# Optimization experiments

Hardware: AMD Instinct MI355X
Metric: run time of the kernel (lower is better)

Reference implementation:

```python
import jax, jax.numpy as jnp
import numpy as np
import math

B = 1024      # graphs
N = 64        # nodes per graph (padded, masked by node_mask)
BN = B * N    # total nodes
EPG = 192     # directed edges per graph
E = B * EPG


def setup_inputs() -> dict:
    key = jax.random.key(0)
    ks = jax.random.split(key, 40)

    def nrm(k, shp, s=0.02):
        return (jax.random.normal(k, shp) * s).astype(jnp.float32)

    mol_batch_x = jax.random.normal(ks[0], (BN, 19), dtype=jnp.float32)
    offs = jnp.arange(B, dtype=jnp.int32) * N
    src = jax.random.randint(ks[1], (B, EPG), 0, N, dtype=jnp.int32) + offs[:, None]
    dst = jax.random.randint(ks[2], (B, EPG), 0, N, dtype=jnp.int32) + offs[:, None]
    mol_batch_edge_index = jnp.stack([src.reshape(-1), dst.reshape(-1)], axis=0)
    mol_batch_batch = jnp.repeat(jnp.arange(B, dtype=jnp.int32), N)
    text_features = jax.random.normal(ks[3], (B, 300), dtype=jnp.float32)
    timesteps = jax.random.uniform(ks[4], (B,), minval=0.0, maxval=1000.0, dtype=jnp.float32)
    node_mask = (jax.random.uniform(ks[5], (B, N)) > 0.1).astype(jnp.float32)

    p = {
        'W_tr': nrm(ks[6], (19, 300)),   'b_tr': jnp.zeros((300,), jnp.float32),
        'W_c1': nrm(ks[7], (300, 600)),  'b_c1': jnp.zeros((600,), jnp.float32),
        'W_c2': nrm(ks[8], (600, 600)),  'b_c2': jnp.zeros((600,), jnp.float32),
        'W_c3': nrm(ks[9], (600, 600)),  'b_c3': jnp.zeros((600,), jnp.float32),
        'W_h1': nrm(ks[10], (600, 600)), 'b_h1': jnp.zeros((600,), jnp.float32),
        'W_h2': nrm(ks[11], (600, 600)), 'b_h2': jnp.zeros((600,), jnp.float32),
        'W_h3': nrm(ks[12], (600, 300)), 'b_h3': jnp.zeros((300,), jnp.float32),
        'ln_g': jnp.ones((300,), jnp.float32), 'ln_b': jnp.zeros((300,), jnp.float32),
        'W_t1': nrm(ks[13], (128, 512)), 'b_t1': jnp.zeros((512,), jnp.float32),
        'W_t2': nrm(ks[14], (512, 512)), 'b_t2': jnp.zeros((512,), jnp.float32),
        'W_e':  nrm(ks[15], (512, 3000)), 'b_e': jnp.zeros((3000,), jnp.float32),
    }
    return dict(mol_batch_x=mol_batch_x, mol_batch_edge_index=mol_batch_edge_index,
                mol_batch_batch=mol_batch_batch, text_features=text_features,
                timesteps=timesteps, node_mask=node_mask, **p)


def timestep_embedding(t, dim=128, max_period=10000.0):
    half = dim // 2
    freqs = jnp.exp(-math.log(max_period) * jnp.arange(half, dtype=jnp.float32) / half)
    args = t[:, None] * freqs[None]                 # [B, half]
    return jnp.concatenate([jnp.cos(args), jnp.sin(args)], axis=-1)  # [B, dim]


def gcn_conv(x, W, b, src, dst, num_nodes):
    # PyG GCNConv: D^{-1/2} (A + I) D^{-1/2} X W + b, edge weights 1
    h = x @ W                                             # [BN, F]
    deg = jnp.zeros((num_nodes,), h.dtype).at[dst].add(1.0) + 1.0  # in-degree + self-loop
    inv_sqrt = jax.lax.rsqrt(deg)
    coef = inv_sqrt[src] * inv_sqrt[dst]                  # [E]
    agg = jax.ops.segment_sum(h[src] * coef[:, None], dst, num_segments=num_nodes)
    return agg + h * (1.0 / deg)[:, None] + b             # self-loop norm = 1/deg


def global_mean_pool(x, batch, num_graphs):
    sums = jax.ops.segment_sum(x, batch, num_segments=num_graphs)
    cnts = jax.ops.segment_sum(jnp.ones((x.shape[0],), x.dtype), batch, num_segments=num_graphs)
    return sums / jnp.maximum(cnts, 1.0)[:, None]


def layer_norm(x, g, b, eps=1e-5):
    mu = jnp.mean(x, axis=-1, keepdims=True)
    var = jnp.mean(jnp.square(x - mu), axis=-1, keepdims=True)
    return (x - mu) * jax.lax.rsqrt(var + eps) * g + b


def reference(mol_batch_x, mol_batch_edge_index, mol_batch_batch, text_features,
              timesteps, node_mask, W_tr, b_tr, W_c1, b_c1, W_c2, b_c2, W_c3, b_c3,
              W_h1, b_h1, W_h2, b_h2, W_h3, b_h3, ln_g, ln_b,
              W_t1, b_t1, W_t2, b_t2, W_e, b_e):
    num_nodes = mol_batch_x.shape[0]
    num_graphs = node_mask.shape[0]
    src, dst = mol_batch_edge_index[0], mol_batch_edge_index[1]

    # FiLM conditioning from timestep embedding
    emb = jax.nn.relu(timestep_embedding(timesteps, 128) @ W_t1 + b_t1) @ W_t2 + b_t2  # [B,512]
    emb_out = jax.nn.relu(emb) @ W_e + b_e                                             # [B,3000]
    s1, t1 = emb_out[:, 0:600], emb_out[:, 600:1200]
    s2, t2 = emb_out[:, 1200:1800], emb_out[:, 1800:2400]
    s3, t3 = emb_out[:, 2400:2700], emb_out[:, 2700:3000]

    # node transform + mask
    x = mol_batch_x @ W_tr + b_tr                     # [BN, 300]
    x = x * node_mask.reshape(-1, 1)

    # GCN stack
    x = jax.nn.relu(gcn_conv(x, W_c1, b_c1, src, dst, num_nodes))
    x = jax.nn.relu(gcn_conv(x, W_c2, b_c2, src, dst, num_nodes))
    x = gcn_conv(x, W_c3, b_c3, src, dst, num_nodes)  # [BN, 600]

    g = global_mean_pool(x, mol_batch_batch, num_graphs)  # [B, 600]
    g = jax.nn.relu(g @ W_h1 + b_h1)
    g = g * (1.0 + s1) + t1
    g = jax.nn.relu(g @ W_h2 + b_h2)
    g = g * (1.0 + s2) + t2
    g = g @ W_h3 + b_h3                                # [B, 300]
    g = g * (1.0 + s3) + t3
    g = layer_norm(g, ln_g, ln_b)
    return (g, text_features)
```

## Files before the change

### kernel.cpp

```cpp
#include <hip/hip_runtime.h>
#include <hip/hip_bf16.h>
#include <cstdint>
#include <cstddef>

static constexpr int B   = 1024;
static constexpr int N   = 64;
static constexpr int BN  = B * N;
static constexpr int EPG = 192;
static constexpr int E   = B * EPG;
static constexpr int FP  = 608;
static constexpr int KP1 = 320;
static constexpr int PMS = 72;
static constexpr int NCONV = 2560;

typedef __hip_bfloat16 bf16;
typedef __bf16 bf16x8 __attribute__((ext_vector_type(8)));
typedef __bf16 bf16x4 __attribute__((ext_vector_type(4)));
typedef float  f32x4  __attribute__((ext_vector_type(4)));

__device__ __forceinline__ void storeC(float* p, float v) { *p = v; }
__device__ __forceinline__ void storeC(bf16* p, float v) { *p = __float2bfloat16(v); }

__device__ __forceinline__ void llds16(const void* g, void* l) {
    __builtin_amdgcn_global_load_lds(
        (const __attribute__((address_space(1))) unsigned int*)g,
        (__attribute__((address_space(3))) unsigned int*)l,
        16, 0, 0);
}


template<bool RELU, bool FILM, typename CT>
__device__ __forceinline__ void g64_tile(
    const bf16* __restrict__ A, int lda,
    const bf16* __restrict__ Bt, int ldb,
    const float* __restrict__ bias,
    CT* __restrict__ C, int ldc, int Ncap,
    const bf16* __restrict__ fS, const bf16* __restrict__ fT, int fstride,
    int K, int m0, int n0, char* lds, int tid)
{
    const int lane = tid & 63;
    const int w    = tid >> 6;
    const int wn   = w * 32;
    const int l15  = lane & 15;
    const int lhi  = lane >> 4;
    const int co   = (lhi ^ ((l15 >> 1) & 3)) << 3;
    const int nk   = K >> 5;

    auto stage = [&](int k0, char* buf) {
        {
            int row = tid >> 2;
            int kc  = (tid & 3) ^ ((row >> 1) & 3);
            llds16(A + (size_t)(m0 + row) * lda + k0 + kc * 8,
                   buf + (size_t)(w * 64) * 16);
        }
        #pragma unroll
        for (int t = 0; t < 2; ++t) {
            int ci  = t * 256 + tid;
            int row = ci >> 2;
            int kc  = (ci & 3) ^ ((row >> 1) & 3);
            llds16(Bt + (size_t)(n0 + row) * ldb + k0 + kc * 8,
                   buf + 4096 + (size_t)(t * 256 + w * 64) * 16);
        }
    };

    f32x4 acc[4][2] = {};
    stage(0, lds);
    asm volatile("s_waitcnt vmcnt(0)" ::: "memory");
    __syncthreads();

    for (int k = 0; k < nk; ++k) {
        if (k + 1 < nk) stage((k + 1) << 5, lds + ((k + 1) & 1) * 12288);

        __bf16* As = (__bf16*)(lds + (k & 1) * 12288);
        __bf16* Bs = As + 2048;
        bf16x8 af[4], bg[2];
        #pragma unroll
        for (int i = 0; i < 4; ++i)
            af[i] = *(bf16x8*)(As + (i * 16 + l15) * 32 + co);
        #pragma unroll
        for (int j = 0; j < 2; ++j)
            bg[j] = *(bf16x8*)(Bs + (wn + j * 16 + l15) * 32 + co);
        #pragma unroll
        for (int i = 0; i < 4; ++i)
            #pragma unroll
            for (int j = 0; j < 2; ++j)
                acc[i][j] = __builtin_amdgcn_mfma_f32_16x16x32_bf16(
                    af[i], bg[j], acc[i][j], 0, 0, 0);

        asm volatile("s_waitcnt vmcnt(0)" ::: "memory");
        __syncthreads();
    }

    #pragma unroll
    for (int i = 0; i < 4; ++i) {
        #pragma unroll
        for (int j = 0; j < 2; ++j) {
            int col = n0 + wn + j * 16 + l15;
            if (col < Ncap) {
                float bv = bias ? bias[col] : 0.f;
                #pragma unroll
                for (int e = 0; e < 4; ++e) {
                    int row = m0 + i * 16 + lhi * 4 + e;
                    float v = acc[i][j][e] + bv;
                    if (RELU) v = fmaxf(v, 0.f);
                    if (FILM) {
                        float sv = __bfloat162float(fS[(size_t)row * fstride + col]);
                        float tv = __bfloat162float(fT[(size_t)row * fstride + col]);
                        v = v * (1.f + sv) + tv;
                    }
                    storeC(&C[(size_t)row * ldc + col], v);
                }
            }
        }
    }
}

__device__ __forceinline__ void g64_tile8(
    const bf16* __restrict__ A, int lda,
    const bf16* __restrict__ Bt, int ldb,
    const float* __restrict__ bias,
    bf16* __restrict__ C, int ldc, int Ncap,
    int K, int m0, int n0, char* lds, int tid)
{
    const int lane = tid & 63;
    const int w    = tid >> 6;
    const int wn   = w * 16;
    const int l15  = lane & 15;
    const int lhi  = lane >> 4;
    const int co   = (lhi ^ ((l15 >> 1) & 3)) << 3;
    const int nk   = K >> 5;

    auto stage = [&](int k0, char* buf) {
        if (tid < 256) {
            int row = tid >> 2;
            int kc  = (tid & 3) ^ ((row >> 1) & 3);
            llds16(A + (size_t)(m0 + row) * lda + k0 + kc * 8,
                   buf + (size_t)(w * 64) * 16);
        }
        {
            int row = tid >> 2;
            int kc  = (tid & 3) ^ ((row >> 1) & 3);
            llds16(Bt + (size_t)(n0 + row) * ldb + k0 + kc * 8,
                   buf + 4096 + (size_t)(w * 64) * 16);
        }
    };

    f32x4 acc[4] = {};
    stage(0, lds);
    asm volatile("s_waitcnt vmcnt(0)" ::: "memory");
    __syncthreads();

    for (int k = 0; k < nk; ++k) {
        if (k + 1 < nk) stage((k + 1) << 5, lds + ((k + 1) & 1) * 12288);

        __bf16* As = (__bf16*)(lds + (k & 1) * 12288);
        __bf16* Bs = As + 2048;
        bf16x8 af[4], bg;
        #pragma unroll
        for (int i = 0; i < 4; ++i)
            af[i] = *(bf16x8*)(As + (i * 16 + l15) * 32 + co);
        bg = *(bf16x8*)(Bs + (wn + l15) * 32 + co);
        #pragma unroll
        for (int i = 0; i < 4; ++i)
            acc[i] = __builtin_amdgcn_mfma_f32_16x16x32_bf16(af[i], bg, acc[i], 0, 0, 0);

        asm volatile("s_waitcnt vmcnt(0)" ::: "memory");
        __syncthreads();
    }

    int col = n0 + wn + l15;
    if (col < Ncap) {
        float bv = bias ? bias[col] : 0.f;
        #pragma unroll
        for (int i = 0; i < 4; ++i)
            #pragma unroll
            for (int e = 0; e < 4; ++e) {
                int row = m0 + i * 16 + lhi * 4 + e;
                float v = fmaxf(acc[i][e] + bv, 0.f);
                C[(size_t)row * ldc + col] = __float2bfloat16(v);
            }
    }
}

__device__ __attribute__((noinline)) void guest_g64(
    const bf16* gA, int glda, const bf16* gBt, int gldb,
    const float* gbias, bf16* gC, int gldc, int gNcap, int gK, int gnt,
    int t, char* lds, int tid)
{
    int mt2 = t / gnt, nt2 = t % gnt;
    g64_tile8(gA, glda, gBt, gldb, gbias, gC, gldc, gNcap,
              gK, mt2 * 64, nt2 * 128, lds, tid);
}

template<bool RELU, bool FILM, typename CT>
__global__ __launch_bounds__(256) void gemm64(
    const bf16* __restrict__ A, int lda,
    const bf16* __restrict__ Bt, int ldb,
    const float* __restrict__ bias,
    CT* __restrict__ C, int ldc, int Ncap,
    const bf16* __restrict__ fS, const bf16* __restrict__ fT, int fstride,
    int K)
{
    __shared__ __align__(16) char lds[24576];
    g64_tile<RELU, FILM, CT>(A, lda, Bt, ldb, bias, C, ldc, Ncap,
                             fS, fT, fstride, K,
                             blockIdx.x * 64, blockIdx.y * 128, lds,
                             threadIdx.x);
}

__global__ __launch_bounds__(256) void k_two_gemms(
    const bf16* __restrict__ A2b, const bf16* __restrict__ Wet,
    const float* __restrict__ b_e, bf16* __restrict__ EO,
    const bf16* __restrict__ Yv, const bf16* __restrict__ Wb3,
    const float* __restrict__ b_c3, bf16* __restrict__ G0)
{
    __shared__ __align__(16) char lds[24576];
    int bid = blockIdx.x;
    if (bid < 384) {
        int mt = bid / 24, nt = bid % 24;
        g64_tile<false, false, bf16>(A2b, 512, Wet, 512, b_e, EO, 3000, 3000,
                                     nullptr, nullptr, 0, 512,
                                     mt * 64, nt * 128, lds, threadIdx.x);
    } else {
        int t = bid - 384;
        int mt = t / 5, nt = t % 5;
        g64_tile<false, false, bf16>(Yv, FP, Wb3, FP, b_c3, G0, FP, 600,
                                     nullptr, nullptr, 0, FP,
                                     mt * 64, nt * 128, lds, threadIdx.x);
    }
}

__global__ __launch_bounds__(512, 6) void conv1_gemm(
    const bf16* __restrict__ A,
    const bf16* __restrict__ Bt,
    const float* __restrict__ bias,
    bf16* __restrict__ X1,
    const bf16* __restrict__ gA, int glda,
    const bf16* __restrict__ gBt, int gldb,
    const float* __restrict__ gbias,
    bf16* __restrict__ gC, int gldc, int gNcap, int gK, int gnt)
{
    __shared__ __align__(16) char regA[32768];
    const int tid = threadIdx.x;
    const int bid = blockIdx.x;

    if (bid >= NCONV) {
        guest_g64(gA, glda, gBt, gldb, gbias, gC, gldc, gNcap, gK, gnt,
                  bid - NCONV, regA, tid);
        return;
    }

    const int lane = tid & 63;
    const int w    = tid >> 6;
    const int wm   = (w & 1) * 64;
    const int wn   = (w >> 1) * 32;
    const int l15  = lane & 15;
    const int lhi  = lane >> 4;
    const int co   = (lhi ^ ((l15 >> 1) & 3)) << 3;

    const int lid = bid >> 3;
    const int mt  = (bid & 7) * 64 + lid / 5;
    const int nt  = lid % 5;
    const int m0  = mt * 128;
    const int n0  = nt * 128;

    auto stage = [&](int k0, char* buf) {
        int row = tid >> 2;
        int kc  = (tid & 3) ^ ((row >> 1) & 3);
        llds16(A  + (size_t)(m0 + row) * KP1 + k0 + kc * 8,
               buf + (size_t)(w * 64) * 16);
        llds16(Bt + (size_t)(n0 + row) * KP1 + k0 + kc * 8,
               buf + 8192 + (size_t)(w * 64) * 16);
    };

    constexpr int nk = KP1 / 32;
    f32x4 acc[4][2] = {};
    stage(0, regA);
    asm volatile("s_waitcnt vmcnt(0)" ::: "memory");
    __syncthreads();

    for (int k = 0; k < nk; ++k) {
        if (k + 1 < nk) stage((k + 1) << 5, regA + ((k + 1) & 1) * 16384);

        __bf16* As = (__bf16*)(regA + (k & 1) * 16384);
        __bf16* Bs = As + 4096;
        bf16x8 af[4], bg[2];
        #pragma unroll
        for (int i = 0; i < 4; ++i)
            af[i] = *(bf16x8*)(As + (wm + i * 16 + l15) * 32 + co);
        #pragma unroll
        for (int j = 0; j < 2; ++j)
            bg[j] = *(bf16x8*)(Bs + (wn + j * 16 + l15) * 32 + co);
        #pragma unroll
        for (int i = 0; i < 4; ++i)
            #pragma unroll
            for (int j = 0; j < 2; ++j)
                acc[i][j] = __builtin_amdgcn_mfma_f32_16x16x32_bf16(
                    af[i], bg[j], acc[i][j], 0, 0, 0);

        asm volatile("s_waitcnt vmcnt(0)" ::: "memory");
        __syncthreads();
    }

    #pragma unroll
    for (int i = 0; i < 4; ++i)
        #pragma unroll
        for (int j = 0; j < 2; ++j) {
            int col = n0 + wn + j * 16 + l15;
            if (col < FP) {
                float bv = (col < 600) ? bias[col] : 0.f;
                #pragma unroll
                for (int e = 0; e < 4; ++e) {
                    int row = m0 + wm + i * 16 + lhi * 4 + e;
                    float v = fmaxf(acc[i][j][e] + bv, 0.f);
                    X1[(size_t)row * FP + col] = __float2bfloat16(v);
                }
            }
        }
}

__global__ __launch_bounds__(512, 6) void conv_fused_q(
    const bf16* __restrict__ A, int lda, int K,
    const bf16* __restrict__ Bt, int ldb,
    const bf16* __restrict__ Pmg,
    const float* __restrict__ bias,
    const float* __restrict__ qv,
    bf16* __restrict__ Y,
    const bf16* __restrict__ gA, int glda,
    const bf16* __restrict__ gBt, int gldb,
    const float* __restrict__ gbias,
    bf16* __restrict__ gC, int gldc, int gNcap, int gK, int gnt)
{
    __shared__ __align__(16) char regA[35840];
    __shared__ float s_q[128];

    const int tid = threadIdx.x;
    const int bid = blockIdx.x;

    if (bid >= NCONV) {
        guest_g64(gA, glda, gBt, gldb, gbias, gC, gldc, gNcap, gK, gnt,
                  bid - NCONV, regA, tid);
        return;
    }

    __bf16* Ts = (__bf16*)regA;
    __bf16* Pm = (__bf16*)(regA + 17408);

    const int lane = tid & 63;
    const int w    = tid >> 6;
    const int wm   = (w & 1) * 64;
    const int wn   = (w >> 1) * 32;
    const int l15  = lane & 15;
    const int lhi  = lane >> 4;
    const int co   = (lhi ^ ((l15 >> 1) & 3)) << 3;

    const int lid = bid >> 3;
    const int mt  = (bid & 7) * 64 + lid / 5;
    const int nt  = lid % 5;
    const int m0  = mt * 128;
    const int n0  = nt * 128;

    if (tid < 128) s_q[tid] = qv[mt * 128 + tid];

    auto stage = [&](int k0, char* buf) {
        int row = tid >> 2;
        int kc  = (tid & 3) ^ ((row >> 1) & 3);
        llds16(A  + (size_t)(m0 + row) * lda + k0 + kc * 8,
               buf + (size_t)(w * 64) * 16);
        llds16(Bt + (size_t)(n0 + row) * ldb + k0 + kc * 8,
               buf + 8192 + (size_t)(w * 64) * 16);
    };

    const int nk = K >> 5;
    f32x4 acc[4][2] = {};
    stage(0, regA);
    asm volatile("s_waitcnt vmcnt(0)" ::: "memory");
    __syncthreads();

    for (int k = 0; k < nk; ++k) {
        if (k + 1 < nk) {
            stage((k + 1) << 5, regA + ((k + 1) & 1) * 16384);
        } else {
            #pragma unroll
            for (int i = 0; i < 2; ++i)
                llds16(Pmg + (size_t)mt * (128 * PMS) + (size_t)(i * 512 + tid) * 8,
                       (char*)Pm + (size_t)(i * 512 + w * 64) * 16);
            if (w < 2)
                llds16(Pmg + (size_t)mt * (128 * PMS) + (size_t)(1024 + w * 64 + lane) * 8,
                       (char*)Pm + (size_t)(1024 + w * 64) * 16);
        }

        __bf16* As = (__bf16*)(regA + (k & 1) * 16384);
        __bf16* Bs = As + 4096;
        bf16x8 af[4], bg[2];
        #pragma unroll
        for (int i = 0; i < 4; ++i)
            af[i] = *(bf16x8*)(As + (wm + i * 16 + l15) * 32 + co);
        #pragma unroll
        for (int j = 0; j < 2; ++j)
            bg[j] = *(bf16x8*)(Bs + (wn + j * 16 + l15) * 32 + co);
        #pragma unroll
        for (int i = 0; i < 4; ++i)
            #pragma unroll
            for (int j = 0; j < 2; ++j)
                acc[i][j] = __builtin_amdgcn_mfma_f32_16x16x32_bf16(
                    af[i], bg[j], acc[i][j], 0, 0, 0);

        asm volatile("s_waitcnt vmcnt(0)" ::: "memory");
        __syncthreads();
    }

    const int g  = w & 1;
    const int nb = w >> 1;
    #pragma unroll
    for (int h = 0; h < 2; ++h) {
        if ((w >> 2) == h) {
            #pragma unroll
            for (int i = 0; i < 4; ++i)
                #pragma unroll
                for (int j = 0; j < 2; ++j) {
                    int c_local = (wn & 63) + j * 16 + l15;
                    int rbase   = wm + i * 16 + lhi * 4;
                    bf16x4 pk;
                    #pragma unroll
                    for (int e = 0; e < 4; ++e) pk[e] = (__bf16)acc[i][j][e];
                    *(bf16x4*)(Ts + c_local * 136 + rbase) = pk;
                }
        }
        __syncthreads();

        f32x4 acc2[4] = {};
        #pragma unroll
        for (int k0 = 0; k0 < 64; k0 += 32) {
            bf16x8 pa[4], hb;
            #pragma unroll
            for (int i = 0; i < 4; ++i)
                pa[i] = *(bf16x8*)(Pm + (g * 64 + i * 16 + l15) * PMS + k0 + lhi * 8);
            hb = *(bf16x8*)(Ts + (nb * 16 + l15) * 136 + g * 64 + k0 + lhi * 8);
            #pragma unroll
            for (int i = 0; i < 4; ++i)
                acc2[i] = __builtin_amdgcn_mfma_f32_16x16x32_bf16(
                    pa[i], hb, acc2[i], 0, 0, 0);
        }
        {
            int col = n0 + h * 64 + nb * 16 + l15;
            float bv = (col < 600) ? bias[col] : 0.f;
            float yp = 0.f;
            #pragma unroll
            for (int i = 0; i < 4; ++i)
                #pragma unroll
                for (int e = 0; e < 4; ++e) {
                    float v = fmaxf(acc2[i][e] + bv, 0.f);
                    yp += s_q[g * 64 + i * 16 + lhi * 4 + e] * v;
                }
            yp += __shfl_xor(yp, 16, 64);
            yp += __shfl_xor(yp, 32, 64);
            if (lhi == 0 && col < FP)
                Y[(size_t)(mt * 2 + g) * FP + col] = __float2bfloat16(yp);
        }
        __syncthreads();
    }
}

struct WtJob  { const float* src; bf16* dst; int Ksrc, Nsrc, Kp, Np, blk0; };
struct PrepArgs {
    WtJob j[9];
    int nwt, te0, pp0, xtr0;
    const int*   ei;
    const float* ts;
    const float* xin; const float* Wtr; const float* btr; const float* mask;
    bf16* TE; bf16* Pmg; float* qv; bf16* PX0;
};

__global__ __launch_bounds__(256) void k_prep(PrepArgs a)
{
    __shared__ __align__(16) char sm[35840];
    const int bx  = blockIdx.x;
    const int tid = threadIdx.x;

    if (bx < a.nwt) {
        int ji = 0;
        while (ji < 8 && bx >= a.j[ji + 1].blk0) ++ji;
        WtJob jb = a.j[ji];
        int t  = bx - jb.blk0;
        int kt = (jb.Kp + 63) >> 6;
        int ti = t % kt, tj = t / kt;
        int kg0 = ti * 64, ng0 = tj * 64;
        float (*T)[65] = (float(*)[65])sm;
        #pragma unroll 4
        for (int r = 0; r < 16; ++r) {
            int kl = (tid >> 6) + r * 4, nl = tid & 63;
            int kg = kg0 + kl, ng = ng0 + nl;
            T[kl][nl] = (kg < jb.Ksrc && ng < jb.Nsrc)
                        ? jb.src[(size_t)kg * jb.Nsrc + ng] : 0.f;
        }
        __syncthreads();
        #pragma unroll 4
        for (int r = 0; r < 16; ++r) {
            int nl = (tid >> 6) + r * 4, kl = tid & 63;
            int ng = ng0 + nl, kg = kg0 + kl;
            if (ng < jb.Np && kg < jb.Kp)
                jb.dst[(size_t)ng * jb.Kp + kg] = __float2bfloat16(T[kl][nl]);
        }
    } else if (bx < a.pp0) {
        int idx = (bx - a.te0) * 256 + tid;
        int b = idx >> 7, jj = idx & 127;
        float tt = a.ts[b];
        int h = jj & 63;
        float freq = expf(-9.210340371976184f * (float)h / 64.f);
        float ang = tt * freq;
        a.TE[idx] = __float2bfloat16((jj < 64) ? cosf(ang) : sinf(ang));
    } else if (bx < a.xtr0) {
        int pr = bx - a.pp0;
        float* Pf   = (float*)sm;
        int*   cnt  = (int*)(sm + 32768);
        float* sQ   = (float*)(sm + 33280);
        float* sI   = (float*)(sm + 33792);
        float* sIvd = (float*)(sm + 34304);

        for (int idx = tid; idx < 8192; idx += 256) Pf[idx] = 0.f;
        if (tid < 128) cnt[tid] = 0;
        __syncthreads();
        for (int e = tid; e < 2 * EPG; e += 256) {
            int g  = (e >= EPG);
            int eg = (2 * pr + g) * EPG + (e - g * EPG);
            int ld = (a.ei[E + eg] & 63) + g * 64;
            atomicAdd(&cnt[ld], 1);
        }
        __syncthreads();
        if (tid < 128) {
            float d = (float)cnt[tid] + 1.0f;
            float iv = 1.f / d;
            sIvd[tid] = iv;
            sI[tid]   = rsqrtf(d);
            sQ[tid]   = iv;
        }
        __syncthreads();
        for (int e = tid; e < 2 * EPG; e += 256) {
            int g   = (e >= EPG);
            int eg  = (2 * pr + g) * EPG + (e - g * EPG);
            int lsl = a.ei[eg] & 63;
            int ldl = a.ei[E + eg] & 63;
            float cf = sI[g * 64 + lsl] * sI[g * 64 + ldl];
            atomicAdd(&Pf[(g * 64 + ldl) * 64 + lsl], cf);
            atomicAdd(&sQ[g * 64 + lsl], cf);
        }
        __syncthreads();
        if (tid < 128) {
            Pf[tid * 64 + (tid & 63)] += sIvd[tid];
            a.qv[pr * 128 + tid] = sQ[tid] * (1.f / 64.f);
        }
        __syncthreads();
        for (int idx = tid; idx < 128 * PMS; idx += 256) {
            int r = idx / PMS, k = idx - r * PMS;
            float v = (k < 64) ? Pf[r * 64 + k] : 0.f;
            a.Pmg[(size_t)pr * (128 * PMS) + idx] = __float2bfloat16(v);
        }
    } else {
        int g = bx - a.xtr0;
        float* Pf  = (float*)sm;
        float* Ws  = (float*)sm;
        float* xm  = (float*)(sm + 23104);
        float* xa  = (float*)(sm + 28224);
        float* isqv= (float*)(sm + 33344);
        float* ivdv= (float*)(sm + 33600);
        int*   cnt = (int*)  (sm + 33856);
        float* sb  = (float*)(sm + 34112);

        for (int idx = tid; idx < 4096; idx += 256) Pf[idx] = 0.f;
        if (tid < 64) cnt[tid] = 0;
        __syncthreads();
        for (int e = tid; e < EPG; e += 256)
            atomicAdd(&cnt[a.ei[E + g * EPG + e] & 63], 1);
        __syncthreads();
        if (tid < 64) {
            float d = (float)cnt[tid] + 1.0f;
            ivdv[tid] = 1.f / d;
            isqv[tid] = rsqrtf(d);
        }
        __syncthreads();
        for (int e = tid; e < EPG; e += 256) {
            int ls = a.ei[g * EPG + e] & 63;
            int ld = a.ei[E + g * EPG + e] & 63;
            atomicAdd(&Pf[ld * 64 + ls], isqv[ls] * isqv[ld]);
        }
        for (int idx = tid; idx < 64 * 20; idx += 256) {
            int n = idx / 20, j = idx - n * 20;
            float mv = a.mask[g * 64 + n];
            xm[idx] = (j < 19) ? mv * a.xin[(size_t)(g * 64 + n) * 19 + j] : mv;
        }
        __syncthreads();
        if (tid < 64) Pf[tid * 64 + tid] += ivdv[tid];
        __syncthreads();
        for (int idx = tid; idx < 64 * 20; idx += 256) {
            int r = idx / 20, j = idx - r * 20;
            float s = 0.f;
            #pragma unroll 8
            for (int s2 = 0; s2 < 64; ++s2)
                s += Pf[r * 64 + s2] * xm[s2 * 20 + j];
            xa[idx] = s;
        }
        __syncthreads();
        for (int idx = tid; idx < 19 * 304; idx += 256) {
            int k = idx / 304, c = idx - k * 304;
            Ws[idx] = (c < 300) ? a.Wtr[k * 300 + c] : 0.f;
        }
        for (int c = tid; c < 304; c += 256)
            sb[c] = (c < 300) ? a.btr[c] : 0.f;
        __syncthreads();
        int n  = tid >> 2;
        int c0 = tid & 3;
        float ba = xa[n * 20 + 19];
        for (int c = c0; c < 304; c += 4) {
            float acc = ba * sb[c];
            #pragma unroll
            for (int k = 0; k < 19; ++k)
                acc += xa[n * 20 + k] * Ws[k * 304 + c];
            a.PX0[(size_t)(g * 64 + n) * KP1 + c] = __float2bfloat16(acc);
        }
        bf16x8 z = {};
        for (int idx = tid; idx < 64 * 2; idx += 256) {
            int nn = idx >> 1, jv = idx & 1;
            *(bf16x8*)((__bf16*)a.PX0 + (size_t)(g * 64 + nn) * KP1 + 304 + jv * 8) = z;
        }
    }
}

__global__ __launch_bounds__(256) void k_ln_copy(const float* __restrict__ G,
                                                 const float* __restrict__ lg,
                                                 const float* __restrict__ lb,
                                                 const float* __restrict__ text,
                                                 float* __restrict__ out)
{
    int r = blockIdx.x;
    int tid = threadIdx.x;
    __shared__ float red[4];
    __shared__ float smu, svar;

    float v0 = (tid < 300) ? G[r * 300 + tid] : 0.f;
    float v1 = (tid + 256 < 300) ? G[r * 300 + tid + 256] : 0.f;
    float s = v0 + v1;
    #pragma unroll
    for (int o = 32; o > 0; o >>= 1) s += __shfl_down(s, o, 64);
    if ((tid & 63) == 0) red[tid >> 6] = s;
    __syncthreads();
    if (tid == 0) smu = (red[0] + red[1] + red[2] + red[3]) * (1.f / 300.f);
    __syncthreads();
    float mu = smu;
    float d0 = (tid < 300) ? v0 - mu : 0.f;
    float d1 = (tid + 256 < 300) ? v1 - mu : 0.f;
    s = d0 * d0 + d1 * d1;
    #pragma unroll
    for (int o = 32; o > 0; o >>= 1) s += __shfl_down(s, o, 64);
    if ((tid & 63) == 0) red[tid >> 6] = s;
    __syncthreads();
    if (tid == 0) svar = (red[0] + red[1] + red[2] + red[3]) * (1.f / 300.f);
    __syncthreads();
    float rstd = rsqrtf(svar + 1e-5f);
    if (tid < 300)
        out[r * 300 + tid] = d0 * rstd * lg[tid] + lb[tid];
    if (tid + 256 < 300)
        out[r * 300 + tid + 256] = d1 * rstd * lg[tid + 256] + lb[tid + 256];
    float* o2 = out + (size_t)B * 300;
    for (int c = tid; c < 300; c += 256)
        o2[(size_t)r * 300 + c] = text[(size_t)r * 300 + c];
}

extern "C" void kernel_launch(void* const* d_in, const int* in_sizes, int n_in,
                              void* d_out, int out_size, void* d_ws, size_t ws_size,
                              hipStream_t stream)
{
    const float* x_in  = (const float*)d_in[0];
    const int*   ei    = (const int*)d_in[1];
    const float* text  = (const float*)d_in[3];
    const float* tst   = (const float*)d_in[4];
    const float* mask  = (const float*)d_in[5];
    const float* W_tr  = (const float*)d_in[6];
    const float* b_tr  = (const float*)d_in[7];
    const float* W_c1  = (const float*)d_in[8];
    const float* b_c1  = (const float*)d_in[9];
    const float* W_c2  = (const float*)d_in[10];
    const float* b_c2  = (const float*)d_in[11];
    const float* W_c3  = (const float*)d_in[12];
    const float* b_c3  = (const float*)d_in[13];
    const float* W_h1  = (const float*)d_in[14];
    const float* b_h1  = (const float*)d_in[15];
    const float* W_h2  = (const float*)d_in[16];
    const float* b_h2  = (const float*)d_in[17];
    const float* W_h3  = (const float*)d_in[18];
    const float* b_h3  = (const float*)d_in[19];
    const float* ln_g  = (const float*)d_in[20];
    const float* ln_b  = (const float*)d_in[21];
    const float* W_t1  = (const float*)d_in[22];
    const float* b_t1  = (const float*)d_in[23];
    const float* W_t2  = (const float*)d_in[24];
    const float* b_t2  = (const float*)d_in[25];
    const float* W_e   = (const float*)d_in[26];
    const float* b_e   = (const float*)d_in[27];

    char* w = (char*)d_ws;
    size_t off = 0;
    auto carve = [&](size_t bytes) {
        void* p = w + off;
        off += (bytes + 255) & ~(size_t)255;
        return p;
    };
    bf16*  PX0    = (bf16*) carve((size_t)BN * KP1 * 2);
    bf16*  X1     = (bf16*) carve((size_t)BN * FP * 2);
    bf16*  Wb1    = (bf16*) carve((size_t)640 * KP1 * 2);
    bf16*  Wb2    = (bf16*) carve((size_t)640 * FP * 2);
    bf16*  Wb3    = (bf16*) carve((size_t)640 * FP * 2);
    bf16*  Wt1t   = (bf16*) carve((size_t)512 * 128 * 2);
    bf16*  Wt2t   = (bf16*) carve((size_t)512 * 512 * 2);
    bf16*  Wet    = (bf16*) carve((size_t)3072 * 512 * 2);
    bf16*  Wh1t   = (bf16*) carve((size_t)640 * FP * 2);
    bf16*  Wh2t   = (bf16*) carve((size_t)640 * FP * 2);
    bf16*  Wh3t   = (bf16*) carve((size_t)384 * FP * 2);
    bf16*  TE     = (bf16*) carve((size_t)B * 128 * 2);
    bf16*  A1b    = (bf16*) carve((size_t)B * 512 * 2);
    bf16*  A2b    = (bf16*) carve((size_t)B * 512 * 2);
    bf16*  EO     = (bf16*) carve((size_t)B * 3000 * 2);
    bf16*  Yv     = (bf16*) carve((size_t)B * FP * 2);
    bf16*  G0     = (bf16*) carve((size_t)B * FP * 2);
    bf16*  G1     = (bf16*) carve((size_t)B * FP * 2);
    bf16*  G2     = (bf16*) carve((size_t)B * FP * 2);
    float* G3     = (float*)carve((size_t)B * 300 * 4);
    bf16*  Pmg    = (bf16*) carve((size_t)512 * 128 * PMS * 2);
    float* qv     = (float*)carve((size_t)BN * 4);
    (void)ws_size; (void)in_sizes; (void)n_in; (void)out_size;

    float* out = (float*)d_out;

    PrepArgs pa;
    struct JD { const float* s; bf16* d; int Ks, Ns, Kp, Np; };
    JD jd[9] = {
        { W_c1, Wb1,  300, 600,  KP1, 640 },
        { W_c2, Wb2,  600, 600,  FP,  640 },
        { W_c3, Wb3,  600, 600,  FP,  640 },
        { W_t1, Wt1t, 128, 512,  128, 512 },
        { W_t2, Wt2t, 512, 512,  512, 512 },
        { W_e,  Wet,  512, 3000, 512, 3072 },
        { W_h1, Wh1t, 600, 600,  FP,  640 },
        { W_h2, Wh2t, 600, 600,  FP,  640 },
        { W_h3, Wh3t, 600, 300,  FP,  384 },
    };
    int cum = 0;
    for (int i = 0; i < 9; ++i) {
        int kt = (jd[i].Kp + 63) >> 6, nt = (jd[i].Np + 63) >> 6;
        pa.j[i] = { jd[i].s, jd[i].d, jd[i].Ks, jd[i].Ns, jd[i].Kp, jd[i].Np, cum };
        cum += kt * nt;
    }
    pa.nwt  = cum;
    pa.te0  = cum;       cum += (B * 128) / 256;
    pa.pp0  = cum;       cum += B / 2;
    pa.xtr0 = cum;       cum += B;
    pa.ei = ei; pa.ts = tst;
    pa.xin = x_in; pa.Wtr = W_tr; pa.btr = b_tr; pa.mask = mask;
    pa.TE = TE; pa.Pmg = Pmg; pa.qv = qv; pa.PX0 = PX0;
    k_prep<<<cum, 256, 0, stream>>>(pa);

    conv1_gemm<<<NCONV + 64, 512, 0, stream>>>(
        PX0, Wb1, b_c1, X1,
        TE, 128, Wt1t, 128, b_t1, A1b, 512, 512, 128, 4);

    conv_fused_q<<<NCONV + 64, 512, 0, stream>>>(
        X1, FP, FP, Wb2, FP, Pmg, b_c2, qv, Yv,
        A1b, 512, Wt2t, 512, b_t2, A2b, 512, 512, 512, 4);

    k_two_gemms<<<464, 256, 0, stream>>>(A2b, Wet, b_e, EO, Yv, Wb3, b_c3, G0);

    gemm64<true, true, bf16><<<dim3(16, 5), 256, 0, stream>>>(
        G0, FP, Wh1t, FP, b_h1, G1, FP, 600, EO + 0, EO + 600, 3000, FP);
    gemm64<true, true, bf16><<<dim3(16, 5), 256, 0, stream>>>(
        G1, FP, Wh2t, FP, b_h2, G2, FP, 600, EO + 1200, EO + 1800, 3000, FP);
    gemm64<false, true, float><<<dim3(16, 3), 256, 0, stream>>>(
        G2, FP, Wh3t, FP, b_h3, G3, 300, 300, EO + 2400, EO + 2700, 3000, FP);

    k_ln_copy<<<B, 256, 0, stream>>>(G3, ln_g, ln_b, text, out);
}
```

Before: 342.4 us.

## Widen conv GEMM tiles to 128x256 and prefetch propagation matrix upfront

The two conv GEMM kernels now use 128x256 output tiles instead of 128x128. Each wave computes a 64x64 sub-tile, and the grid shrinks from 2560 to 1536 conv blocks over three N-tiles. The propagation-matrix tile is loaded into its own LDS region at kernel start rather than during the last K iteration, and the conv1/conv2 weights are padded to 768 columns to match. The intent is to raise MFMA work per LDS load and cut redundant A-tile traffic, at the cost of larger LDS and register use, lower occupancy (launch bounds 6 to 4), and wasted compute on padded columns (768 vs 608).

```diff
diff --git a/kernel.cpp b/kernel.cpp
--- a/kernel.cpp
+++ b/kernel.cpp
@@ -11,7 +11,7 @@
 static constexpr int FP  = 608;
 static constexpr int KP1 = 320;
 static constexpr int PMS = 72;
-static constexpr int NCONV = 2560;
+static constexpr int NCONV = 1536;
 
 typedef __hip_bfloat16 bf16;
 typedef __bf16 bf16x8 __attribute__((ext_vector_type(8)));
@@ -230,7 +230,7 @@
     }
 }
 
-__global__ __launch_bounds__(512, 6) void conv1_gemm(
+__global__ __launch_bounds__(512, 4) void conv1_gemm(
     const bf16* __restrict__ A,
     const bf16* __restrict__ Bt,
     const float* __restrict__ bias,
@@ -240,7 +240,7 @@
     const float* __restrict__ gbias,
     bf16* __restrict__ gC, int gldc, int gNcap, int gK, int gnt)
 {
-    __shared__ __align__(16) char regA[32768];
+    __shared__ __align__(16) char regA[49152];
     const int tid = threadIdx.x;
     const int bid = blockIdx.x;
 
@@ -253,48 +253,58 @@
     const int lane = tid & 63;
     const int w    = tid >> 6;
     const int wm   = (w & 1) * 64;
-    const int wn   = (w >> 1) * 32;
+    const int wn   = (w >> 1) * 64;
     const int l15  = lane & 15;
     const int lhi  = lane >> 4;
     const int co   = (lhi ^ ((l15 >> 1) & 3)) << 3;
 
     const int lid = bid >> 3;
-    const int mt  = (bid & 7) * 64 + lid / 5;
-    const int nt  = lid % 5;
+    const int mt  = (bid & 7) * 64 + lid / 3;
+    const int nt  = lid % 3;
     const int m0  = mt * 128;
-    const int n0  = nt * 128;
+    const int n0  = nt * 256;
 
     auto stage = [&](int k0, char* buf) {
-        int row = tid >> 2;
-        int kc  = (tid & 3) ^ ((row >> 1) & 3);
-        llds16(A  + (size_t)(m0 + row) * KP1 + k0 + kc * 8,
-               buf + (size_t)(w * 64) * 16);
-        llds16(Bt + (size_t)(n0 + row) * KP1 + k0 + kc * 8,
-               buf + 8192 + (size_t)(w * 64) * 16);
+        #pragma unroll
+        for (int r = 0; r < 3; ++r) {
+            int ci = r * 512 + tid;
+            const bf16* src;
+            if (r == 0) {
+                int row = ci >> 2;
+                int kc  = (ci & 3) ^ ((row >> 1) & 3);
+                src = A + (size_t)(m0 + row) * KP1 + k0 + kc * 8;
+            } else {
+                int bi  = ci - 512;
+                int row = bi >> 2;
+                int kc  = (bi & 3) ^ ((row >> 1) & 3);
+                src = Bt + (size_t)(n0 + row) * KP1 + k0 + kc * 8;
+            }
+            llds16(src, buf + (size_t)(r * 512 + w * 64) * 16);
+        }
     };
 
     constexpr int nk = KP1 / 32;
-    f32x4 acc[4][2] = {};
+    f32x4 acc[4][4] = {};
     stage(0, regA);
     asm volatile("s_waitcnt vmcnt(0)" ::: "memory");
     __syncthreads();
 
     for (int k = 0; k < nk; ++k) {
-        if (k + 1 < nk) stage((k + 1) << 5, regA + ((k + 1) & 1) * 16384);
-
-        __bf16* As = (__bf16*)(regA + (k & 1) * 16384);
+        if (k + 1 < nk) stage((k + 1) << 5, regA + ((k + 1) & 1) * 24576);
+
+        __bf16* As = (__bf16*)(regA + (k & 1) * 24576);
         __bf16* Bs = As + 4096;
-        bf16x8 af[4], bg[2];
+        bf16x8 af[4], bg[4];
         #pragma unroll
         for (int i = 0; i < 4; ++i)
             af[i] = *(bf16x8*)(As + (wm + i * 16 + l15) * 32 + co);
         #pragma unroll
-        for (int j = 0; j < 2; ++j)
+        for (int j = 0; j < 4; ++j)
             bg[j] = *(bf16x8*)(Bs + (wn + j * 16 + l15) * 32 + co);
         #pragma unroll
         for (int i = 0; i < 4; ++i)
             #pragma unroll
-            for (int j = 0; j < 2; ++j)
+            for (int j = 0; j < 4; ++j)
                 acc[i][j] = __builtin_amdgcn_mfma_f32_16x16x32_bf16(
                     af[i], bg[j], acc[i][j], 0, 0, 0);
 
@@ -305,7 +315,7 @@
     #pragma unroll
     for (int i = 0; i < 4; ++i)
         #pragma unroll
-        for (int j = 0; j < 2; ++j) {
+        for (int j = 0; j < 4; ++j) {
             int col = n0 + wn + j * 16 + l15;
             if (col < FP) {
                 float bv = (col < 600) ? bias[col] : 0.f;
@@ -319,7 +329,7 @@
         }
 }
 
-__global__ __launch_bounds__(512, 6) void conv_fused_q(
+__global__ __launch_bounds__(512, 4) void conv_fused_q(
     const bf16* __restrict__ A, int lda, int K,
     const bf16* __restrict__ Bt, int ldb,
     const bf16* __restrict__ Pmg,
@@ -331,9 +341,7 @@
     const float* __restrict__ gbias,
     bf16* __restrict__ gC, int gldc, int gNcap, int gK, int gnt)
 {
-    __shared__ __align__(16) char regA[35840];
-    __shared__ float s_q[128];
-
+    __shared__ __align__(16) char regA[68096];
     const int tid = threadIdx.x;
     const int bid = blockIdx.x;
 
@@ -343,66 +351,76 @@
         return;
     }
 
-    __bf16* Ts = (__bf16*)regA;
-    __bf16* Pm = (__bf16*)(regA + 17408);
+    __bf16* Ts  = (__bf16*)regA;
+    __bf16* Pm  = (__bf16*)(regA + 49152);
+    float*  s_q = (float*)(regA + 67584);
 
     const int lane = tid & 63;
     const int w    = tid >> 6;
     const int wm   = (w & 1) * 64;
-    const int wn   = (w >> 1) * 32;
+    const int wn   = (w >> 1) * 64;
     const int l15  = lane & 15;
     const int lhi  = lane >> 4;
     const int co   = (lhi ^ ((l15 >> 1) & 3)) << 3;
 
     const int lid = bid >> 3;
-    const int mt  = (bid & 7) * 64 + lid / 5;
-    const int nt  = lid % 5;
+    const int mt  = (bid & 7) * 64 + lid / 3;
+    const int nt  = lid % 3;
     const int m0  = mt * 128;
-    const int n0  = nt * 128;
+    const int n0  = nt * 256;
 
     if (tid < 128) s_q[tid] = qv[mt * 128 + tid];
 
+    {
+        const bf16* ps = Pmg + (size_t)mt * (128 * PMS);
+        llds16(ps + (size_t)tid * 8,          regA + 49152 + (size_t)(w * 64) * 16);
+        llds16(ps + (size_t)(512 + tid) * 8,  regA + 49152 + (size_t)(512 + w * 64) * 16);
+        if (tid < 128)
+            llds16(ps + (size_t)(1024 + tid) * 8,
+                   regA + 49152 + (size_t)(1024 + w * 64) * 16);
+    }
+
     auto stage = [&](int k0, char* buf) {
-        int row = tid >> 2;
-        int kc  = (tid & 3) ^ ((row >> 1) & 3);
-        llds16(A  + (size_t)(m0 + row) * lda + k0 + kc * 8,
-               buf + (size_t)(w * 64) * 16);
-        llds16(Bt + (size_t)(n0 + row) * ldb + k0 + kc * 8,
-               buf + 8192 + (size_t)(w * 64) * 16);
+        #pragma unroll
+        for (int r = 0; r < 3; ++r) {
+            int ci = r * 512 + tid;
+            const bf16* src;
+            if (r == 0) {
+                int row = ci >> 2;
+                int kc  = (ci & 3) ^ ((row >> 1) & 3);
+                src = A + (size_t)(m0 + row) * lda + k0 + kc * 8;
+            } else {
+                int bi  = ci - 512;
+                int row = bi >> 2;
+                int kc  = (bi & 3) ^ ((row >> 1) & 3);
+                src = Bt + (size_t)(n0 + row) * ldb + k0 + kc * 8;
+            }
+            llds16(src, buf + (size_t)(r * 512 + w * 64) * 16);
+        }
     };
 
     const int nk = K >> 5;
-    f32x4 acc[4][2] = {};
+    f32x4 acc[4][4] = {};
     stage(0, regA);
     asm volatile("s_waitcnt vmcnt(0)" ::: "memory");
     __syncthreads();
 
     for (int k = 0; k < nk; ++k) {
-        if (k + 1 < nk) {
-            stage((k + 1) << 5, regA + ((k + 1) & 1) * 16384);
-        } else {
+        if (k + 1 < nk) stage((k + 1) << 5, regA + ((k + 1) & 1) * 24576);
+
+        __bf16* As = (__bf16*)(regA + (k & 1) * 24576);
+        __bf16* Bs = As + 4096;
+        bf16x8 af[4], bg[4];
+        #pragma unroll
+        for (int i = 0; i < 4; ++i)
+            af[i] = *(bf16x8*)(As + (wm + i * 16 + l15) * 32 + co);
+        #pragma unroll
+        for (int j = 0; j < 4; ++j)
+            bg[j] = *(bf16x8*)(Bs + (wn + j * 16 + l15) * 32 + co);
+        #pragma unroll
+        for (int i = 0; i < 4; ++i)
             #pragma unroll
-            for (int i = 0; i < 2; ++i)
-                llds16(Pmg + (size_t)mt * (128 * PMS) + (size_t)(i * 512 + tid) * 8,
-                       (char*)Pm + (size_t)(i * 512 + w * 64) * 16);
-            if (w < 2)
-                llds16(Pmg + (size_t)mt * (128 * PMS) + (size_t)(1024 + w * 64 + lane) * 8,
-                       (char*)Pm + (size_t)(1024 + w * 64) * 16);
-        }
-
-        __bf16* As = (__bf16*)(regA + (k & 1) * 16384);
-        __bf16* Bs = As + 4096;
-        bf16x8 af[4], bg[2];
-        #pragma unroll
-        for (int i = 0; i < 4; ++i)
-            af[i] = *(bf16x8*)(As + (wm + i * 16 + l15) * 32 + co);
-        #pragma unroll
-        for (int j = 0; j < 2; ++j)
-            bg[j] = *(bf16x8*)(Bs + (wn + j * 16 + l15) * 32 + co);
-        #pragma unroll
-        for (int i = 0; i < 4; ++i)
-            #pragma unroll
-            for (int j = 0; j < 2; ++j)
+            for (int j = 0; j < 4; ++j)
                 acc[i][j] = __builtin_amdgcn_mfma_f32_16x16x32_bf16(
                     af[i], bg[j], acc[i][j], 0, 0, 0);
 
@@ -410,16 +428,15 @@
         __syncthreads();
     }
 
-    const int g  = w & 1;
-    const int nb = w >> 1;
+    const int f = w;
     #pragma unroll
     for (int h = 0; h < 2; ++h) {
         if ((w >> 2) == h) {
             #pragma unroll
             for (int i = 0; i < 4; ++i)
                 #pragma unroll
-                for (int j = 0; j < 2; ++j) {
-                    int c_local = (wn & 63) + j * 16 + l15;
+                for (int j = 0; j < 4; ++j) {
+                    int c_local = (wn & 127) + j * 16 + l15;
                     int rbase   = wm + i * 16 + lhi * 4;
                     bf16x4 pk;
                     #pragma unroll
@@ -429,21 +446,22 @@
         }
         __syncthreads();
 
-        f32x4 acc2[4] = {};
-        #pragma unroll
-        for (int k0 = 0; k0 < 64; k0 += 32) {
-            bf16x8 pa[4], hb;
+        #pragma unroll
+        for (int g2 = 0; g2 < 2; ++g2) {
+            f32x4 acc2[4] = {};
             #pragma unroll
-            for (int i = 0; i < 4; ++i)
-                pa[i] = *(bf16x8*)(Pm + (g * 64 + i * 16 + l15) * PMS + k0 + lhi * 8);
-            hb = *(bf16x8*)(Ts + (nb * 16 + l15) * 136 + g * 64 + k0 + lhi * 8);
-            #pragma unroll
-            for (int i = 0; i < 4; ++i)
-                acc2[i] = __builtin_amdgcn_mfma_f32_16x16x32_bf16(
-                    pa[i], hb, acc2[i], 0, 0, 0);
-        }
-        {
-            int col = n0 + h * 64 + nb * 16 + l15;
+            for (int k0 = 0; k0 < 64; k0 += 32) {
+                bf16x8 pa[4], hb;
+                #pragma unroll
+                for (int i = 0; i < 4; ++i)
+                    pa[i] = *(bf16x8*)(Pm + (g2 * 64 + i * 16 + l15) * PMS + k0 + lhi * 8);
+                hb = *(bf16x8*)(Ts + (f * 16 + l15) * 136 + g2 * 64 + k0 + lhi * 8);
+                #pragma unroll
+                for (int i = 0; i < 4; ++i)
+                    acc2[i] = __builtin_amdgcn_mfma_f32_16x16x32_bf16(
+                        pa[i], hb, acc2[i], 0, 0, 0);
+            }
+            int col = n0 + h * 128 + f * 16 + l15;
             float bv = (col < 600) ? bias[col] : 0.f;
             float yp = 0.f;
             #pragma unroll
@@ -451,12 +469,12 @@
                 #pragma unroll
                 for (int e = 0; e < 4; ++e) {
                     float v = fmaxf(acc2[i][e] + bv, 0.f);
-                    yp += s_q[g * 64 + i * 16 + lhi * 4 + e] * v;
+                    yp += s_q[g2 * 64 + i * 16 + lhi * 4 + e] * v;
                 }
             yp += __shfl_xor(yp, 16, 64);
             yp += __shfl_xor(yp, 32, 64);
             if (lhi == 0 && col < FP)
-                Y[(size_t)(mt * 2 + g) * FP + col] = __float2bfloat16(yp);
+                Y[(size_t)(mt * 2 + g2) * FP + col] = __float2bfloat16(yp);
         }
         __syncthreads();
     }
@@ -707,8 +725,8 @@
     };
     bf16*  PX0    = (bf16*) carve((size_t)BN * KP1 * 2);
     bf16*  X1     = (bf16*) carve((size_t)BN * FP * 2);
-    bf16*  Wb1    = (bf16*) carve((size_t)640 * KP1 * 2);
-    bf16*  Wb2    = (bf16*) carve((size_t)640 * FP * 2);
+    bf16*  Wb1    = (bf16*) carve((size_t)768 * KP1 * 2);
+    bf16*  Wb2    = (bf16*) carve((size_t)768 * FP * 2);
     bf16*  Wb3    = (bf16*) carve((size_t)640 * FP * 2);
     bf16*  Wt1t   = (bf16*) carve((size_t)512 * 128 * 2);
     bf16*  Wt2t   = (bf16*) carve((size_t)512 * 512 * 2);
@@ -734,8 +752,8 @@
     PrepArgs pa;
     struct JD { const float* s; bf16* d; int Ks, Ns, Kp, Np; };
     JD jd[9] = {
-        { W_c1, Wb1,  300, 600,  KP1, 640 },
-        { W_c2, Wb2,  600, 600,  FP,  640 },
+        { W_c1, Wb1,  300, 600,  KP1, 768 },
+        { W_c2, Wb2,  600, 600,  FP,  768 },
         { W_c3, Wb3,  600, 600,  FP,  640 },
         { W_t1, Wt1t, 128, 512,  128, 512 },
         { W_t2, Wt2t, 512, 512,  512, 512 },
```

New measurement: 349.4 us. +2.1%, slower.
